# Performance work log

Hardware: AMD Instinct MI355X
Metric: run time of the kernel (lower is better)

## Reference

```python
import jax, jax.numpy as jnp
import numpy as np
from jax import lax

HID = 2048; NK = 16; NV = 32; DK = 128; DV = 128; KSZ = 4; CHUNK = 64; S = 2048
KEY_DIM = NK * DK; VAL_DIM = NV * DV; CONV_DIM = 2 * KEY_DIM + VAL_DIM
EPS = 1e-6


def l2norm(x, eps=1e-6):
    return x * lax.rsqrt((x * x).sum(-1, keepdims=True) + eps)


def chunk_gated_delta_rule(q, k, v, g, beta, chunk=CHUNK):
    # q,k: [B,S,Hv,DK]; v: [B,S,Hv,DV]; g,beta: [B,S,Hv]
    q = l2norm(q); k = l2norm(k)  # use_qk_l2norm_in_kernel=True
    q, k, v = (jnp.swapaxes(x, 1, 2) for x in (q, k, v))  # [B,H,S,D]
    g = jnp.swapaxes(g, 1, 2); beta = jnp.swapaxes(beta, 1, 2)  # [B,H,S]
    B, H, Ssz, Dk = k.shape; Dv = v.shape[-1]
    N = Ssz // chunk  # seq_len chosen divisible by chunk -> pad is no-op
    q = q * (Dk ** -0.5)
    vb = v * beta[..., None]
    kb = k * beta[..., None]
    rs = lambda x: x.reshape(B, H, N, chunk, x.shape[-1])
    q, k, v, kb, vb = map(rs, (q, k, v, kb, vb))
    g = jnp.cumsum(g.reshape(B, H, N, chunk), axis=-1)
    tril = jnp.tril(jnp.ones((chunk, chunk), bool))
    stril = jnp.tril(jnp.ones((chunk, chunk), bool), -1)
    diff = jnp.where(tril, g[..., :, None] - g[..., None, :], 0.0)
    decay_mask = jnp.where(tril, jnp.exp(diff), 0.0)  # [B,H,N,C,C]
    attn = jnp.where(stril, -(kb @ jnp.swapaxes(k, -1, -2)) * decay_mask, 0.0)
    # UT (WY) transform: sequential row updates, scan over in-chunk index
    def ut_body(a, i):
        row = jnp.take(a, i, axis=-2)  # [B,H,N,C]
        new = row + jnp.einsum('bhnk,bhnkj->bhnj', row, a)
        return a.at[:, :, :, i, :].set(new), None
    attn, _ = lax.scan(ut_body, attn, jnp.arange(1, chunk))
    attn = attn + jnp.eye(chunk, dtype=attn.dtype)
    u = attn @ vb                                   # [B,H,N,C,DV]
    kcd = attn @ (kb * jnp.exp(g)[..., None])       # [B,H,N,C,DK]
    init = jnp.zeros((B, H, Dk, Dv), q.dtype)
    def step(state, inp):
        q_i, k_i, u_i, kcd_i, g_i, dm_i = inp
        scores = (q_i @ jnp.swapaxes(k_i, -1, -2)) * dm_i
        v_new = u_i - kcd_i @ state
        inter = (q_i * jnp.exp(g_i)[..., None]) @ state
        o = inter + scores @ v_new
        gl = g_i[..., -1]  # [B,H]
        state = state * jnp.exp(gl)[..., None, None] + jnp.einsum(
            'bhcd,bhce->bhde', k_i * jnp.exp(gl[..., None] - g_i)[..., None], v_new)
        return state, o
    mv = lambda x: jnp.moveaxis(x, 2, 0)
    _, out = lax.scan(step, init, (mv(q), mv(k), mv(u), mv(kcd), mv(g), mv(decay_mask)))
    out = jnp.moveaxis(out, 0, 2).reshape(B, H, Ssz, Dv)
    return jnp.swapaxes(out, 1, 2)  # [B,S,H,DV]


def setup_inputs() -> dict:
    key = jax.random.key(0)
    ks = jax.random.split(key, 8)
    return {
        'hidden_states': jax.random.normal(ks[0], (S, HID), jnp.float32),
        'W_qkv': jax.random.normal(ks[1], (CONV_DIM, HID), jnp.float32) * 0.02,
        'W_z': jax.random.normal(ks[2], (VAL_DIM, HID), jnp.float32) * 0.02,
        'W_a': jax.random.normal(ks[3], (NV, HID), jnp.float32) * 0.02,
        'W_b': jax.random.normal(ks[4], (NV, HID), jnp.float32) * 0.02,
        'conv_w': jax.random.normal(ks[5], (CONV_DIM, 1, KSZ), jnp.float32) * 0.1,
        'dt_bias': jnp.ones((NV,), jnp.float32),
        'A_log': jnp.log(jax.random.uniform(ks[6], (NV,), jnp.float32, 0.1, 16.0)),
        'norm_w': jnp.ones((DV,), jnp.float32),
        'W_out': jax.random.normal(ks[7], (HID, VAL_DIM), jnp.float32) * 0.02,
    }


def reference(hidden_states, W_qkv, W_z, W_a, W_b, conv_w, dt_bias, A_log, norm_w, W_out):
    x = hidden_states  # [S, HID]
    mixed = x @ W_qkv.T  # [S, CONV_DIM]
    z = (x @ W_z.T).reshape(-1, DV)  # [S*NV, DV]
    a = x @ W_a.T  # [S, NV]
    b = x @ W_b.T
    # causal depthwise conv1d (torch pads K-1 both sides then slices [:S])
    conv = lax.conv_general_dilated(
        mixed.T[None], conv_w, (1,), [(KSZ - 1, 0)],
        dimension_numbers=('NCH', 'OIH', 'NCH'), feature_group_count=CONV_DIM)
    mixed = jax.nn.silu(conv[0].T)  # [S, CONV_DIM]
    q = mixed[:, :KEY_DIM].reshape(1, S, NK, DK)
    k = mixed[:, KEY_DIM:2 * KEY_DIM].reshape(1, S, NK, DK)
    v = mixed[:, 2 * KEY_DIM:].reshape(1, S, NV, DV)
    beta = jax.nn.sigmoid(b)[None]  # [1,S,NV]
    g = (-jnp.exp(A_log) * jax.nn.softplus(a + dt_bias))[None]  # [1,S,NV]
    ratio = NV // NK
    q = jnp.repeat(q, ratio, axis=2)
    k = jnp.repeat(k, ratio, axis=2)
    core = chunk_gated_delta_rule(q, k, v, g, beta)  # [1,S,NV,DV]
    h = core.reshape(-1, DV)  # [S*NV, DV]
    var = jnp.mean(h * h, axis=-1, keepdims=True)
    h = h * lax.rsqrt(var + EPS) * norm_w
    h = h * jax.nn.silu(z)
    out = h.reshape(S, VAL_DIM) @ W_out.T  # [S, HID]
    return out
```

## Files before the change

### kernel.cpp

```cpp
#include <hip/hip_runtime.h>
#include <hip/hip_bf16.h>
#include <math.h>

#define S_LEN   2048
#define HIDDIM  2048
#define NKH     16
#define NVH     32
#define DKD     128
#define DVD     128
#define CCH     64
#define NCHK    32
#define KEY_DIM 2048
#define VAL_DIM 4096
#define CONV_DIM 8192

#define PA_LDS_BYTES (16384 + 16384 + 32768 + 4096 + 4096 + 256 + 256 + 256)
#define PB_LDS_BYTES ((2 * 29696 + 2048 + 1024 + 1024) * 2 + 2048 * 4)
#define G256_LDS_BYTES (3 * 16384 * 2)
#define G128_LDS_BYTES (3 * 8192 * 2)

typedef __bf16 bf16x8 __attribute__((ext_vector_type(8)));
typedef float f32x4 __attribute__((ext_vector_type(4)));

__device__ __forceinline__ float sigmoid_f(float x) { return 1.f / (1.f + __expf(-x)); }
__device__ __forceinline__ float silu_f(float x) { return x * sigmoid_f(x); }
__device__ __forceinline__ ushort f2bf(float f) {
    unsigned u = __float_as_uint(f);
    u += 0x7fffu + ((u >> 16) & 1u);
    return (ushort)(u >> 16);
}
__device__ __forceinline__ float bf2f(ushort u) {
    return __uint_as_float((unsigned)u << 16);
}

#define GLL(srcp, dstp) __builtin_amdgcn_global_load_lds( \
    (const __attribute__((address_space(1))) void*)(srcp), \
    (__attribute__((address_space(3))) void*)(dstp), 16, 0, 0)

#define NX8  (S_LEN * HIDDIM / 8)
#define NQ8  (CONV_DIM * HIDDIM / 8)
#define NZ8  (VAL_DIM * HIDDIM / 8)
#define NW8  (HIDDIM * VAL_DIM / 8)
__global__ __launch_bounds__(256) void cast4_kernel(
    const float* __restrict__ x, const float* __restrict__ Wq,
    const float* __restrict__ Wz, const float* __restrict__ Wo,
    ushort* __restrict__ xb, ushort* __restrict__ wqz, ushort* __restrict__ wob)
{
    int t = blockIdx.x * 256 + threadIdx.x;
    const float* src;
    ushort* dst;
    if (t < NX8) { src = x + (size_t)t * 8; dst = xb + (size_t)t * 8; }
    else if (t < NX8 + NQ8) {
        size_t o = (size_t)(t - NX8) * 8;
        src = Wq + o; dst = wqz + o;
    } else if (t < NX8 + NQ8 + NZ8) {
        size_t o = (size_t)(t - NX8 - NQ8) * 8;
        src = Wz + o; dst = wqz + (size_t)NQ8 * 8 + o;
    } else {
        size_t o = (size_t)(t - NX8 - NQ8 - NZ8) * 8;
        src = Wo + o; dst = wob + o;
    }
    float4 v0 = *(const float4*)(src);
    float4 v1 = *(const float4*)(src + 4);
    union { ushort u[8]; uint4 v; } r;
    r.u[0] = f2bf(v0.x); r.u[1] = f2bf(v0.y); r.u[2] = f2bf(v0.z); r.u[3] = f2bf(v0.w);
    r.u[4] = f2bf(v1.x); r.u[5] = f2bf(v1.y); r.u[6] = f2bf(v1.z); r.u[7] = f2bf(v1.w);
    *(uint4*)dst = r.v;
}

__global__ __launch_bounds__(256) void cast_ab_kernel(
    const float* __restrict__ Wa, const float* __restrict__ Wb, ushort* __restrict__ out)
{
    int t = blockIdx.x * 256 + threadIdx.x;
    int row = t >> 8;
    int c8 = (t & 255) * 8;
    union { ushort u[8]; uint4 v; } r;
    if (row < 64) {
        const float* src = (row < 32) ? (Wa + (size_t)row * HIDDIM + c8)
                                      : (Wb + (size_t)(row - 32) * HIDDIM + c8);
        float4 v0 = *(const float4*)(src);
        float4 v1 = *(const float4*)(src + 4);
        r.u[0] = f2bf(v0.x); r.u[1] = f2bf(v0.y); r.u[2] = f2bf(v0.z); r.u[3] = f2bf(v0.w);
        r.u[4] = f2bf(v1.x); r.u[5] = f2bf(v1.y); r.u[6] = f2bf(v1.z); r.u[7] = f2bf(v1.w);
    } else {
        r.u[0] = r.u[1] = r.u[2] = r.u[3] = r.u[4] = r.u[5] = r.u[6] = r.u[7] = 0;
    }
    *(uint4*)(out + (size_t)t * 8) = r.v;
}

__global__ __launch_bounds__(512, 1) void gemm256_kernel(
    const ushort* __restrict__ A, const ushort* __restrict__ B,
    ushort* __restrict__ C0, ushort* __restrict__ C1,
    int K, int NSPLIT, int ldc0, int ldc1)
{
    extern __shared__ ushort g2s[];
    const int tid = threadIdx.x;
    const int wv = tid >> 6, ln = tid & 63;
    const int wm = wv >> 1, wn = wv & 1;
    const int lrow = ln & 15, lkg = ln >> 4;
    const int bm = blockIdx.y * 256, bn = blockIdx.x * 256;

    int soff[2];
#pragma unroll
    for (int j = 0; j < 2; ++j) {
        int g = tid + j * 512;
        int l = g & 63;
        soff[j] = (((g >> 6) * 16) + (l & 15)) * K + (l >> 4) * 8;
    }
    const ushort* Abase = A + (size_t)bm * K;
    const ushort* Bbase = B + (size_t)bn * K;

    f32x4 acc[4][8];
#pragma unroll
    for (int m = 0; m < 4; ++m)
#pragma unroll
        for (int n = 0; n < 8; ++n) {
            f32x4 z = {0.f, 0.f, 0.f, 0.f};
            acc[m][n] = z;
        }

#define G256_STAGE(bb, k0) do {                                            \
        ushort* bufA_ = g2s + (bb) * 16384;                                \
        ushort* bufB_ = bufA_ + 8192;                                      \
        _Pragma("unroll")                                                  \
        for (int j_ = 0; j_ < 2; ++j_) {                                   \
            GLL(Abase + soff[j_] + (k0), bufA_ + (j_ * 512 + wv * 64) * 8);\
            GLL(Bbase + soff[j_] + (k0), bufB_ + (j_ * 512 + wv * 64) * 8);\
        }                                                                  \
    } while (0)

    const int T = K >> 5;
    G256_STAGE(0, 0);
    G256_STAGE(1, 32);
    int bb = 0;
    for (int t = 0; t < T; ++t) {
        if (t + 1 < T) {
            asm volatile("s_waitcnt vmcnt(4)" ::: "memory");
        } else {
            asm volatile("s_waitcnt vmcnt(0)" ::: "memory");
        }
        __builtin_amdgcn_s_barrier();
        if (t + 2 < T) G256_STAGE((bb >= 1) ? (bb - 1) : (bb + 2), (t + 2) * 32);
        const ushort* LA = g2s + bb * 16384;
        const ushort* LB = LA + 8192;
        __builtin_amdgcn_s_setprio(1);
        {
            bf16x8 afv[4], bfv[8];
#pragma unroll
            for (int mf = 0; mf < 4; ++mf)
                afv[mf] = *(const bf16x8*)&LA[((wm * 4 + mf) * 64 + ln) * 8];
#pragma unroll
            for (int nf = 0; nf < 8; ++nf)
                bfv[nf] = *(const bf16x8*)&LB[((wn * 8 + nf) * 64 + ln) * 8];
#pragma unroll
            for (int mf = 0; mf < 4; ++mf)
#pragma unroll
                for (int nf = 0; nf < 8; ++nf)
                    acc[mf][nf] = __builtin_amdgcn_mfma_f32_16x16x32_bf16(
                        afv[mf], bfv[nf], acc[mf][nf], 0, 0, 0);
        }
        __builtin_amdgcn_s_setprio(0);
        bb = (bb == 2) ? 0 : bb + 1;
    }
#undef G256_STAGE

    const bool inC1 = (bn >= NSPLIT);
    ushort* Cp = inC1 ? C1 : C0;
    const int ldc = inC1 ? ldc1 : ldc0;
    const int cboff = bn + wn * 128 - (inC1 ? NSPLIT : 0);
#pragma unroll
    for (int mf = 0; mf < 4; ++mf) {
        const int row0 = bm + wm * 64 + mf * 16 + lkg * 4;
#pragma unroll
        for (int nf = 0; nf < 8; ++nf) {
            ushort* cp = Cp + (size_t)row0 * ldc + cboff + nf * 16 + lrow;
#pragma unroll
            for (int j = 0; j < 4; ++j) cp[(size_t)j * ldc] = f2bf(acc[mf][nf][j]);
        }
    }
}

__global__ __launch_bounds__(256, 2) void gemm128_kernel(
    const ushort* __restrict__ A, const ushort* __restrict__ B,
    float* __restrict__ C, int N, int K)
{
    extern __shared__ ushort g1s[];
    const int tid = threadIdx.x;
    const int wv = tid >> 6, ln = tid & 63;
    const int wm = wv >> 1, wn = wv & 1;
    const int lrow = ln & 15, lkg = ln >> 4;
    const int bm = blockIdx.y * 128, bn = blockIdx.x * 128;

    int soff[2];
#pragma unroll
    for (int j = 0; j < 2; ++j) {
        int g = tid + j * 256;
        int l = g & 63;
        soff[j] = (((g >> 6) * 16) + (l & 15)) * K + (l >> 4) * 8;
    }
    const ushort* Abase = A + (size_t)bm * K;
    const ushort* Bbase = B + (size_t)bn * K;

    f32x4 acc[4][4];
#pragma unroll
    for (int m = 0; m < 4; ++m)
#pragma unroll
        for (int n = 0; n < 4; ++n) {
            f32x4 z = {0.f, 0.f, 0.f, 0.f};
            acc[m][n] = z;
        }

#define G128_STAGE(bb, k0) do {                                            \
        ushort* bufA_ = g1s + (bb) * 8192;                                 \
        ushort* bufB_ = bufA_ + 4096;                                      \
        _Pragma("unroll")                                                  \
        for (int j_ = 0; j_ < 2; ++j_) {                                   \
            GLL(Abase + soff[j_] + (k0), bufA_ + (j_ * 256 + wv * 64) * 8);\
            GLL(Bbase + soff[j_] + (k0), bufB_ + (j_ * 256 + wv * 64) * 8);\
        }                                                                  \
    } while (0)

    const int T = K >> 5;
    G128_STAGE(0, 0);
    G128_STAGE(1, 32);
    int bb = 0;
    for (int t = 0; t < T; ++t) {
        if (t + 1 < T) {
            asm volatile("s_waitcnt vmcnt(4)" ::: "memory");
        } else {
            asm volatile("s_waitcnt vmcnt(0)" ::: "memory");
        }
        __builtin_amdgcn_s_barrier();
        if (t + 2 < T) G128_STAGE((bb >= 1) ? (bb - 1) : (bb + 2), (t + 2) * 32);
        const ushort* LA = g1s + bb * 8192;
        const ushort* LB = LA + 4096;
        __builtin_amdgcn_s_setprio(1);
        {
            bf16x8 afv[4], bfv[4];
#pragma unroll
            for (int mf = 0; mf < 4; ++mf)
                afv[mf] = *(const bf16x8*)&LA[((wm * 4 + mf) * 64 + ln) * 8];
#pragma unroll
            for (int nf = 0; nf < 4; ++nf)
                bfv[nf] = *(const bf16x8*)&LB[((wn * 4 + nf) * 64 + ln) * 8];
#pragma unroll
            for (int mf = 0; mf < 4; ++mf)
#pragma unroll
                for (int nf = 0; nf < 4; ++nf)
                    acc[mf][nf] = __builtin_amdgcn_mfma_f32_16x16x32_bf16(
                        afv[mf], bfv[nf], acc[mf][nf], 0, 0, 0);
        }
        __builtin_amdgcn_s_setprio(0);
        bb = (bb == 2) ? 0 : bb + 1;
    }
#undef G128_STAGE

#pragma unroll
    for (int mf = 0; mf < 4; ++mf) {
        const int row0 = bm + wm * 64 + mf * 16 + lkg * 4;
#pragma unroll
        for (int nf = 0; nf < 4; ++nf) {
            float* cp = C + (size_t)row0 * N + bn + wn * 64 + nf * 16 + lrow;
#pragma unroll
            for (int j = 0; j < 4; ++j) cp[(size_t)j * N] = acc[mf][nf][j];
        }
    }
}

__global__ __launch_bounds__(256) void front_kernel(
    const ushort* __restrict__ pre, const float* __restrict__ cw,
    ushort* __restrict__ qnb, ushort* __restrict__ knb, ushort* __restrict__ vbuf)
{
    __shared__ float stage[4096];
    __shared__ float sums[32];
    __shared__ float scal[32];
    const int s = blockIdx.x;
    const int tid = threadIdx.x;

#pragma unroll
    for (int cg = 0; cg < 8; ++cg) {
        const int c = cg * 1024 + tid * 4;
        float w[4][4];
#pragma unroll
        for (int j = 0; j < 4; ++j) {
            float4 wj = *(const float4*)(cw + (size_t)(c + j) * 4);
            w[j][0] = wj.x; w[j][1] = wj.y; w[j][2] = wj.z; w[j][3] = wj.w;
        }
        float a0 = 0.f, a1 = 0.f, a2 = 0.f, a3 = 0.f;
#pragma unroll
        for (int t = 0; t < 4; ++t) {
            int ss = s - 3 + t;
            if (ss >= 0) {
                uint2 xv = *(const uint2*)(pre + (size_t)ss * CONV_DIM + c);
                a0 = fmaf(bf2f((ushort)xv.x), w[0][t], a0);
                a1 = fmaf(bf2f((ushort)(xv.x >> 16)), w[1][t], a1);
                a2 = fmaf(bf2f((ushort)xv.y), w[2][t], a2);
                a3 = fmaf(bf2f((ushort)(xv.y >> 16)), w[3][t], a3);
            }
        }
        a0 = silu_f(a0); a1 = silu_f(a1); a2 = silu_f(a2); a3 = silu_f(a3);
        if (cg < 4) {
            float4 v4 = make_float4(a0, a1, a2, a3);
            *(float4*)&stage[c] = v4;
            float ss2 = a0 * a0 + a1 * a1 + a2 * a2 + a3 * a3;
#pragma unroll
            for (int m = 1; m < 32; m <<= 1) ss2 += __shfl_xor(ss2, m, 32);
            if ((tid & 31) == 0) sums[c >> 7] = ss2;
        } else {
            union { ushort u2[4]; uint2 v; } p;
            p.u2[0] = f2bf(a0); p.u2[1] = f2bf(a1);
            p.u2[2] = f2bf(a2); p.u2[3] = f2bf(a3);
            *(uint2*)(vbuf + (size_t)s * VAL_DIM + (c - 4096)) = p.v;
        }
    }
    __syncthreads();
    if (tid < 32) {
        float sc = rsqrtf(sums[tid] + 1e-6f);
        if (tid < 16) sc *= 0.08838834764831843f;
        scal[tid] = sc;
    }
    __syncthreads();
#pragma unroll
    for (int j = 0; j < 4; ++j) {
        const int c = j * 1024 + tid * 4;
        float4 v4 = *(const float4*)&stage[c];
        const float sc = scal[c >> 7];
        union { ushort u2[4]; uint2 v; } p;
        p.u2[0] = f2bf(v4.x * sc); p.u2[1] = f2bf(v4.y * sc);
        p.u2[2] = f2bf(v4.z * sc); p.u2[3] = f2bf(v4.w * sc);
        if (c < 2048)
            *(uint2*)(qnb + ((size_t)(s * NKH + (c >> 7))) * DKD + (c & 127)) = p.v;
        else
            *(uint2*)(knb + ((size_t)(s * NKH + ((c >> 7) - 16))) * DKD + (c & 127)) = p.v;
    }
}

__global__ __launch_bounds__(256) void gb_kernel(
    const float* __restrict__ ab, const float* __restrict__ dt_bias,
    const float* __restrict__ A_log, float* __restrict__ g, float* __restrict__ beta)
{
    int idx = blockIdx.x * 256 + threadIdx.x;
    int s = idx >> 5, h = idx & 31;
    float av = ab[(size_t)s * 128 + h] + dt_bias[h];
    float sp = (av > 20.f) ? av : log1pf(__expf(av));
    g[idx] = -__expf(A_log[h]) * sp;
    beta[idx] = sigmoid_f(ab[(size_t)s * 128 + 32 + h]);
}

__global__ __launch_bounds__(256) void phaseA_kernel(
    const ushort* __restrict__ qnb, const ushort* __restrict__ knb,
    const ushort* __restrict__ vbuf, const float* __restrict__ gbuf,
    const float* __restrict__ betabuf,
    ushort* __restrict__ u, ushort* __restrict__ kcd,
    ushort* __restrict__ scores, float* __restrict__ gcs_out,
    ushort* __restrict__ knT)
{
    extern __shared__ char pasm[];
    ushort* kb    = (ushort*)(pasm);
    ushort* qb    = (ushort*)(pasm + 16384);
    ushort* Xb    = (ushort*)(pasm + 32768);
    float*  Adiag = (float*)(pasm + 65536);
    ushort* Ab    = (ushort*)(pasm + 69632);
    float*  gcs_s = (float*)(pasm + 73728);
    float*  bet_s = (float*)(pasm + 73984);
    float*  scK_s = (float*)(pasm + 74240);
    float*  Pf    = (float*)qb;

    const int n = blockIdx.x, h = blockIdx.y, kh = h >> 1;
    const int tid = threadIdx.x;
    const int s0 = n * CCH;
    const int wv = tid >> 6, ln = tid & 63;
    const int lrow = ln & 15, lkg = ln >> 4;

    float xr[64];
    if (tid < 128) {
        const ushort* vp = vbuf + (size_t)s0 * VAL_DIM + h * DVD + tid;
#pragma unroll
        for (int i = 0; i < 64; ++i) xr[i] = bf2f(vp[(size_t)i * VAL_DIM]);
    } else {
        const ushort* kp = knb + ((size_t)s0 * NKH + kh) * DKD + (tid - 128);
#pragma unroll
        for (int i = 0; i < 64; ++i) xr[i] = bf2f(kp[(size_t)i * (NKH * DKD)]);
    }

    {
        uint4 z = {0, 0, 0, 0};
#pragma unroll
        for (int i = 0; i < 8; ++i)
            *(uint4*)&Xb[(i * 256 + tid) * 8] = z;
        *(uint4*)&Ab[tid * 8] = z;
    }

    if (tid < 64) {
        float gv = gbuf[(size_t)(s0 + tid) * NVH + h];
#pragma unroll
        for (int off = 1; off < 64; off <<= 1) {
            float pv = __shfl_up(gv, off, 64);
            if (tid >= off) gv += pv;
        }
        float bv = betabuf[(size_t)(s0 + tid) * NVH + h];
        gcs_s[tid] = gv;
        bet_s[tid] = bv;
        scK_s[tid] = bv * __expf(gv);
        gcs_out[(size_t)h * S_LEN + s0 + tid] = gv;
    }

    {
        const int r = tid >> 2, c0 = (tid & 3) * 32;
        const int mbase = (((r >> 4) * 4 + (tid & 3)) * 64 + (r & 15)) * 8;
        const ushort* ksrc = knb + ((size_t)(s0 + r) * NKH + kh) * DKD + c0;
        const ushort* qsrc = qnb + ((size_t)(s0 + r) * NKH + kh) * DKD + c0;
#pragma unroll
        for (int j0 = 0; j0 < 4; ++j0) {
            *(uint4*)&kb[mbase + (j0 << 7)] = *(const uint4*)(ksrc + j0 * 8);
            *(uint4*)&qb[mbase + (j0 << 7)] = *(const uint4*)(qsrc + j0 * 8);
        }
    }
    __syncthreads();

    f32x4 accA[4], accQ[4];
#pragma unroll
    for (int j = 0; j < 4; ++j) {
        f32x4 z = {0.f, 0.f, 0.f, 0.f};
        accA[j] = z; accQ[j] = z;
    }
#pragma unroll
    for (int ks = 0; ks < 4; ++ks) {
        bf16x8 a_k = *(const bf16x8*)&kb[((wv * 4 + ks) * 64 + ln) * 8];
        bf16x8 a_q = *(const bf16x8*)&qb[((wv * 4 + ks) * 64 + ln) * 8];
#pragma unroll
        for (int j = 0; j < 4; ++j) {
            bf16x8 b_k = *(const bf16x8*)&kb[((j * 4 + ks) * 64 + ln) * 8];
            accA[j] = __builtin_amdgcn_mfma_f32_16x16x32_bf16(a_k, b_k, accA[j], 0, 0, 0);
            accQ[j] = __builtin_amdgcn_mfma_f32_16x16x32_bf16(a_q, b_k, accQ[j], 0, 0, 0);
        }
    }
    {
        ushort* scp = scores + (size_t)(h * NCHK + n) * (CCH * CCH);
#pragma unroll
        for (int j = 0; j < 4; ++j) {
            const int c = j * 16 + lrow;
            const float gc = gcs_s[c];
#pragma unroll
            for (int jj = 0; jj < 4; ++jj) {
                const int i = wv * 16 + lkg * 4 + jj;
                const float e = __expf(gcs_s[i] - gc);
                float sv = (i >= c) ? (accQ[j][jj] * e) : 0.f;
                scp[i * CCH + c] = f2bf(sv);
                float aval = (i > c) ? (-bet_s[i] * accA[j][jj] * e) : 0.f;
                if (j == wv) {
                    Adiag[wv * 256 + (i & 15) * 16 + lrow] = aval;
                } else if (j < wv) {
                    const int f = (wv == 1) ? 0 : ((wv == 2) ? 1 : (2 + (j >> 1)));
                    const int lk = ((j & 1) << 4) | lrow;
                    const int lane2 = (i & 15) | ((lk >> 3) << 4);
                    Ab[(f * 64 + lane2) * 8 + (lk & 7)] = f2bf(aval);
                }
            }
        }
    }
    if (tid < 128) {
#pragma unroll
        for (int i4 = 0; i4 < 16; ++i4) {
            float4 b4 = *(const float4*)&bet_s[i4 * 4];
            xr[i4 * 4 + 0] *= b4.x; xr[i4 * 4 + 1] *= b4.y;
            xr[i4 * 4 + 2] *= b4.z; xr[i4 * 4 + 3] *= b4.w;
        }
    } else {
#pragma unroll
        for (int i4 = 0; i4 < 16; ++i4) {
            float4 b4 = *(const float4*)&scK_s[i4 * 4];
            xr[i4 * 4 + 0] *= b4.x; xr[i4 * 4 + 1] *= b4.y;
            xr[i4 * 4 + 2] *= b4.z; xr[i4 * 4 + 3] *= b4.w;
        }
    }
    __syncthreads();

    const int ct = tid >> 4, lct = tid & 15;
#pragma unroll
    for (int s = 0; s < 4; ++s) {
        float y[16];
        float pr[16];
        if (s > 0) {
#pragma unroll
            for (int r = 0; r < 16; ++r) pr[r] = Pf[r * 256 + tid];
        } else {
#pragma unroll
            for (int r = 0; r < 16; ++r) pr[r] = 0.f;
        }
#pragma unroll
        for (int r = 0; r < 16; ++r) {
            float acc = xr[s * 16 + r] + pr[r];
#pragma unroll
            for (int k4 = 0; k4 < 16; k4 += 4) {
                if (k4 < r) {
                    float4 a4 = *(const float4*)&Adiag[s * 256 + r * 16 + k4];
                    if (k4 + 0 < r) acc = fmaf(a4.x, y[k4 + 0], acc);
                    if (k4 + 1 < r) acc = fmaf(a4.y, y[k4 + 1], acc);
                    if (k4 + 2 < r) acc = fmaf(a4.z, y[k4 + 2], acc);
                    if (k4 + 3 < r) acc = fmaf(a4.w, y[k4 + 3], acc);
                }
            }
            y[r] = acc;
        }
        if (tid < 128) {
            ushort* up = u + (size_t)(h * NCHK + n) * (CCH * DVD) + (s * 16) * DVD + tid;
#pragma unroll
            for (int r = 0; r < 16; ++r) up[r * DVD] = f2bf(y[r]);
        } else {
            ushort* kp = kcd + (size_t)(h * NCHK + n) * (CCH * DKD) + (s * 16) * DKD + (tid - 128);
#pragma unroll
            for (int r = 0; r < 16; ++r) kp[r * DKD] = f2bf(y[r]);
        }
        if (s < 3) {
#pragma unroll
            for (int half = 0; half < 2; ++half) {
                union { ushort us[8]; uint4 v; } p;
#pragma unroll
                for (int e = 0; e < 8; ++e) p.us[e] = f2bf(y[half * 8 + e]);
                const int kg = (s & 1) * 2 + half;
                *(uint4*)&Xb[(((s >> 1) * 16 + ct) * 64 + (kg * 16 + lct)) * 8] = p.v;
            }
            __syncthreads();
            const int snx = s + 1;
            const int nT2 = (snx + 1) >> 1;
            f32x4 accP[4];
#pragma unroll
            for (int ctl = 0; ctl < 4; ++ctl) {
                f32x4 z = {0.f, 0.f, 0.f, 0.f};
                accP[ctl] = z;
            }
#pragma unroll
            for (int t2 = 0; t2 < 2; ++t2) {
                if (t2 < nT2) {
                    const int f = (snx == 1) ? 0 : ((snx == 2) ? 1 : (2 + t2));
                    bf16x8 a = *(const bf16x8*)&Ab[(f * 64 + ln) * 8];
#pragma unroll
                    for (int ctl = 0; ctl < 4; ++ctl) {
                        bf16x8 b = *(const bf16x8*)&Xb[((t2 * 16 + wv * 4 + ctl) * 64 + ln) * 8];
                        accP[ctl] = __builtin_amdgcn_mfma_f32_16x16x32_bf16(a, b, accP[ctl], 0, 0, 0);
                    }
                }
            }
#pragma unroll
            for (int ctl = 0; ctl < 4; ++ctl)
#pragma unroll
                for (int jj = 0; jj < 4; ++jj)
                    Pf[(lkg * 4 + jj) * 256 + wv * 64 + ctl * 16 + lrow] = accP[ctl][jj];
            __syncthreads();
        }
    }

    if (!(h & 1)) {
        const int dk = tid >> 1, ch = (tid & 1) * 32;
        ushort* dst = knT + ((size_t)(kh * NCHK + n) * DKD + dk) * CCH + ch;
        const int kpart = ((dk >> 5) * 64) * 8 + (((dk >> 3) & 3) << 4) * 8 + (dk & 7);
#pragma unroll
        for (int j0 = 0; j0 < 32; j0 += 8) {
            union { ushort us[8]; uint4 v; } p;
#pragma unroll
            for (int j = 0; j < 8; ++j) {
                const int row = ch + j0 + j;
                p.us[j] = kb[((row >> 4) * 4 * 64 + (row & 15)) * 8 + kpart];
            }
            *(uint4*)(dst + j0) = p.v;
        }
    }
}

__global__ __launch_bounds__(256) void phaseB_kernel(
    const ushort* __restrict__ qnb, const ushort* __restrict__ knT,
    const ushort* __restrict__ u, const ushort* __restrict__ kcd,
    const ushort* __restrict__ sc, const float* __restrict__ gcs,
    ushort* __restrict__ obuf)
{
    extern __shared__ ushort smu[];
    ushort* storg  = smu + 59392;
    ushort* vnorg  = smu + 61440;
    ushort* vnsorg = smu + 62464;
    float*  gcsall = (float*)(smu + 63488);

    const int h = blockIdx.x;
    const int dvb = blockIdx.y;
    const int d0 = dvb * 16;
    const int kh = h >> 1;
    const int tid = threadIdx.x;
    const int wv = tid >> 6, ln = tid & 63;
    const int lrow = ln & 15, lkg = ln >> 4;

    {
        uint4 z = {0, 0, 0, 0};
        *(uint4*)&storg[tid * 8] = z;
    }

    const int q_lane  = lrow * (NKH * DKD) + kh * DKD + wv * 32 + lkg * 8;
    const int kc_lane = lrow * DKD + wv * 32 + lkg * 8;
    const int st_lane = ((tid >> 7) * 16 + lrow) * 64 + ((tid >> 6) & 1) * 32 + lkg * 8;
    const int dst_e   = wv * 512;

#define PBSTG(bsel, nn) do {                                                  \
        const ushort* qsrc_  = qnb + (size_t)((nn) * CCH) * (NKH * DKD);      \
        const ushort* kcsrc_ = kcd + (size_t)(h * NCHK + (nn)) * (CCH * DKD); \
        const ushort* scsrc_ = sc  + (size_t)(h * NCHK + (nn)) * (CCH * CCH); \
        const ushort* kTsrc_ = knT + (size_t)(kh * NCHK + (nn)) * (DKD * CCH);\
        const ushort* usrc_  = u   + (size_t)(h * NCHK + (nn)) * (CCH * DVD) + d0; \
        ushort* base_ = smu + (bsel) * 29696;                                 \
        _Pragma("unroll")                                                     \
        for (int r_ = 0; r_ < 4; ++r_) {                                      \
            GLL(qsrc_ + q_lane + r_ * 32768, base_ + r_ * 2048 + dst_e);      \
            GLL(kcsrc_ + kc_lane + r_ * 2048, base_ + 8192 + r_ * 2048 + dst_e); \
            GLL(kTsrc_ + st_lane + r_ * 2048, base_ + 20480 + r_ * 2048 + dst_e); \
        }                                                                     \
        _Pragma("unroll")                                                     \
        for (int r_ = 0; r_ < 2; ++r_)                                        \
            GLL(scsrc_ + st_lane + r_ * 2048, base_ + 16384 + r_ * 2048 + dst_e); \
        if (tid < 128)                                                        \
            GLL(usrc_ + (tid >> 1) * DVD + (tid & 1) * 8, base_ + 28672 + tid * 8); \
    } while (0)

    PBSTG(0, 0);
    {
        float4 g0 = *(const float4*)(gcs + (size_t)h * S_LEN + tid * 8);
        float4 g1 = *(const float4*)(gcs + (size_t)h * S_LEN + tid * 8 + 4);
        *(float4*)&gcsall[tid * 8] = g0;
        *(float4*)&gcsall[tid * 8 + 4] = g1;
    }
    __syncthreads();

    f32x4 accS0 = {0.f, 0.f, 0.f, 0.f}, accS1 = {0.f, 0.f, 0.f, 0.f};

    for (int n = 0; n < NCHK; ++n) {
        const int cur = n & 1;
        if (n + 1 < NCHK) PBSTG(cur ^ 1, n + 1);
        const ushort* qorg  = smu + cur * 29696;
        const ushort* kcorg = qorg + 8192;
        const ushort* scorg = qorg + 16384;
        const ushort* kTorg = qorg + 20480;
        const ushort* uorg  = qorg + 28672;
        const float*  gcs_s = gcsall + n * 64;
        const int s0 = n * CCH;

        f32x4 accv = {0.f, 0.f, 0.f, 0.f};
        f32x4 acco = {0.f, 0.f, 0.f, 0.f};
#pragma unroll
        for (int ks = 0; ks < 4; ++ks) {
            bf16x8 b_st = *(const bf16x8*)&storg[(ks * 64 + ln) * 8];
            bf16x8 a_kc = *(const bf16x8*)&kcorg[((wv * 4 + ks) * 64 + ln) * 8];
            bf16x8 a_q  = *(const bf16x8*)&qorg[((wv * 4 + ks) * 64 + ln) * 8];
            accv = __builtin_amdgcn_mfma_f32_16x16x32_bf16(a_kc, b_st, accv, 0, 0, 0);
            acco = __builtin_amdgcn_mfma_f32_16x16x32_bf16(a_q, b_st, acco, 0, 0, 0);
        }
        const int row = wv * 16 + lkg * 4;
        float u0 = bf2f(uorg[(row + 0) * 16 + lrow]);
        float u1 = bf2f(uorg[(row + 1) * 16 + lrow]);
        float u2 = bf2f(uorg[(row + 2) * 16 + lrow]);
        float u3 = bf2f(uorg[(row + 3) * 16 + lrow]);
        const float gl = gcs_s[63];
        float vn0 = u0 - accv[0], vn1 = u1 - accv[1];
        float vn2 = u2 - accv[2], vn3 = u3 - accv[3];
        {
            float g0 = gcs_s[row], g1 = gcs_s[row + 1], g2 = gcs_s[row + 2], g3 = gcs_s[row + 3];
            acco[0] *= __expf(g0); acco[1] *= __expf(g1);
            acco[2] *= __expf(g2); acco[3] *= __expf(g3);
            const int eb = ((wv >> 1) * 64 + ((wv & 1) * 2 + (lkg >> 1)) * 16 + lrow) * 8
                         + (lkg & 1) * 4;
            union { ushort u2a[4]; uint2 v; } pa, pb;
            pa.u2a[0] = f2bf(vn0); pa.u2a[1] = f2bf(vn1);
            pa.u2a[2] = f2bf(vn2); pa.u2a[3] = f2bf(vn3);
            pb.u2a[0] = f2bf(vn0 * __expf(gl - g0)); pb.u2a[1] = f2bf(vn1 * __expf(gl - g1));
            pb.u2a[2] = f2bf(vn2 * __expf(gl - g2)); pb.u2a[3] = f2bf(vn3 * __expf(gl - g3));
            *(uint2*)&vnorg[eb] = pa.v;
            *(uint2*)&vnsorg[eb] = pb.v;
        }
        __syncthreads();

#pragma unroll
        for (int ks = 0; ks < 2; ++ks) {
            bf16x8 a_sc = *(const bf16x8*)&scorg[((wv * 2 + ks) * 64 + ln) * 8];
            bf16x8 b_vn = *(const bf16x8*)&vnorg[(ks * 64 + ln) * 8];
            acco = __builtin_amdgcn_mfma_f32_16x16x32_bf16(a_sc, b_vn, acco, 0, 0, 0);
        }
        ushort* op = obuf + (size_t)(s0 + row) * VAL_DIM + h * DVD + d0 + lrow;
        op[0] = f2bf(acco[0]); op[VAL_DIM] = f2bf(acco[1]);
        op[2 * VAL_DIM] = f2bf(acco[2]); op[3 * VAL_DIM] = f2bf(acco[3]);

        const float egl = __expf(gl);
        accS0 *= egl; accS1 *= egl;
#pragma unroll
        for (int ks = 0; ks < 2; ++ks) {
            bf16x8 a_vs = *(const bf16x8*)&vnsorg[(ks * 64 + ln) * 8];
            bf16x8 b_k0 = *(const bf16x8*)&kTorg[(((wv * 2 + 0) * 2 + ks) * 64 + ln) * 8];
            bf16x8 b_k1 = *(const bf16x8*)&kTorg[(((wv * 2 + 1) * 2 + ks) * 64 + ln) * 8];
            accS0 = __builtin_amdgcn_mfma_f32_16x16x32_bf16(a_vs, b_k0, accS0, 0, 0, 0);
            accS1 = __builtin_amdgcn_mfma_f32_16x16x32_bf16(a_vs, b_k1, accS1, 0, 0, 0);
        }
#pragma unroll
        for (int j = 0; j < 4; ++j) {
            storg[(wv * 64 + ((lrow >> 3)) * 16 + lkg * 4 + j) * 8 + (lrow & 7)] = f2bf(accS0[j]);
            storg[(wv * 64 + (2 + (lrow >> 3)) * 16 + lkg * 4 + j) * 8 + (lrow & 7)] = f2bf(accS1[j]);
        }
        __syncthreads();
    }
#undef PBSTG
}

__global__ __launch_bounds__(256) void norm_kernel(
    const ushort* __restrict__ obuf, const ushort* __restrict__ z,
    const float* __restrict__ nw, ushort* __restrict__ hbuf)
{
    int row = (blockIdx.x * 256 + threadIdx.x) >> 6;
    int lane = threadIdx.x & 63;
    uint ov = *(const uint*)(obuf + (size_t)row * DVD + lane * 2);
    float x0 = bf2f((ushort)ov), x1 = bf2f((ushort)(ov >> 16));
    float ss = x0 * x0 + x1 * x1;
#pragma unroll
    for (int m = 1; m < 64; m <<= 1) ss += __shfl_xor(ss, m, 64);
    float scale = rsqrtf(ss * (1.f / DVD) + 1e-6f);
    uint zv = *(const uint*)(z + (size_t)row * DVD + lane * 2);
    float z0 = bf2f((ushort)zv), z1 = bf2f((ushort)(zv >> 16));
    float2 w2 = *(const float2*)(nw + lane * 2);
    float h0 = x0 * scale * w2.x * silu_f(z0);
    float h1 = x1 * scale * w2.y * silu_f(z1);
    union { ushort u[2]; uint v; } r;
    r.u[0] = f2bf(h0); r.u[1] = f2bf(h1);
    *(uint*)(hbuf + (size_t)row * DVD + lane * 2) = r.v;
}

extern "C" void kernel_launch(void* const* d_in, const int* in_sizes, int n_in,
                              void* d_out, int out_size, void* d_ws, size_t ws_size,
                              hipStream_t stream)
{
    (void)in_sizes; (void)n_in; (void)out_size; (void)ws_size;
    const float* x      = (const float*)d_in[0];
    const float* W_qkv  = (const float*)d_in[1];
    const float* W_z    = (const float*)d_in[2];
    const float* W_a    = (const float*)d_in[3];
    const float* W_b    = (const float*)d_in[4];
    const float* conv_w = (const float*)d_in[5];
    const float* dt_b   = (const float*)d_in[6];
    const float* A_log  = (const float*)d_in[7];
    const float* norm_w = (const float*)d_in[8];
    const float* W_out  = (const float*)d_in[9];
    float* out = (float*)d_out;

    char* ws = (char*)d_ws;
    ushort* mixed_pre = (ushort*)(ws);
    ushort* u_buf     = (ushort*)(ws);
    ushort* kcd_buf   = (ushort*)(ws + 33554432);
    ushort* knT_buf   = (ushort*)(ws + 50331648);
    ushort* wqz       = (ushort*)(ws + 67108864);
    ushort* xb        = (ushort*)(ws + 117440512);
    ushort* vbuf      = (ushort*)(ws + 67108864);
    ushort* obuf      = (ushort*)(ws + 83886080);
    ushort* hbuf      = (ushort*)(ws + 100663296);
    ushort* z_buf     = (ushort*)(ws + 134217728);
    ushort* sc_buf    = (ushort*)(ws + 167772160);
    ushort* wabb      = (ushort*)(ws + 167772160);
    float*  ab_buf    = (float*)(ws + 168296448);
    ushort* qnb       = (ushort*)(ws + 176160768);
    ushort* knb       = (ushort*)(ws + 184549376);
    float*  g_buf     = (float*)(ws + 201326592);
    float*  bet_buf   = (float*)(ws + 201588736);
    float*  gcs_buf   = (float*)(ws + 201850880);
    ushort* wob       = (ushort*)(ws + 202113024);

    hipFuncSetAttribute((const void*)phaseA_kernel,
                        hipFuncAttributeMaxDynamicSharedMemorySize, PA_LDS_BYTES);
    hipFuncSetAttribute((const void*)phaseB_kernel,
                        hipFuncAttributeMaxDynamicSharedMemorySize, PB_LDS_BYTES);
    hipFuncSetAttribute((const void*)gemm256_kernel,
                        hipFuncAttributeMaxDynamicSharedMemorySize, G256_LDS_BYTES);
    hipFuncSetAttribute((const void*)gemm128_kernel,
                        hipFuncAttributeMaxDynamicSharedMemorySize, G128_LDS_BYTES);

    dim3 blk(256);
    cast4_kernel<<<(NX8 + NQ8 + NZ8 + NW8) / 256, blk, 0, stream>>>(
        x, W_qkv, W_z, W_out, xb, wqz, wob);
    cast_ab_kernel<<<(128 * HIDDIM / 8) / 256, blk, 0, stream>>>(W_a, W_b, wabb);
    gemm256_kernel<<<dim3((CONV_DIM + VAL_DIM) / 256, S_LEN / 256), dim3(512), G256_LDS_BYTES, stream>>>(
        xb, wqz, mixed_pre, z_buf, HIDDIM, CONV_DIM, CONV_DIM, VAL_DIM);
    gemm128_kernel<<<dim3(1, S_LEN / 128), blk, G128_LDS_BYTES, stream>>>(
        xb, wabb, ab_buf, 128, HIDDIM);
    front_kernel<<<S_LEN, blk, 0, stream>>>(mixed_pre, conv_w, qnb, knb, vbuf);
    gb_kernel<<<(S_LEN * NVH) / 256, blk, 0, stream>>>(ab_buf, dt_b, A_log, g_buf, bet_buf);
    phaseA_kernel<<<dim3(NCHK, NVH), blk, PA_LDS_BYTES, stream>>>(
        qnb, knb, vbuf, g_buf, bet_buf, u_buf, kcd_buf, sc_buf, gcs_buf, knT_buf);
    phaseB_kernel<<<dim3(NVH, 8), blk, PB_LDS_BYTES, stream>>>(
        qnb, knT_buf, u_buf, kcd_buf, sc_buf, gcs_buf, obuf);
    norm_kernel<<<(S_LEN * NVH * 64) / 256, blk, 0, stream>>>(obuf, z_buf, norm_w, hbuf);
    gemm128_kernel<<<dim3(HIDDIM / 128, S_LEN / 128), blk, G128_LDS_BYTES, stream>>>(
        hbuf, wob, out, HIDDIM, VAL_DIM);
}
```

Before: 440.9 us.

## Fold a/b projection into big QKVZ GEMM and merge cast kernels

The W_a/W_b casts are folded into the main cast kernel, and the a/b projection is appended as an extra 256-column tile to the large QKVZ GEMM. That GEMM gains a third fp32 output region and a block-index swizzle over the 49x8 grid. This removes two kernel launches and the small, poorly occupied 128-wide GEMM. The cost is zero-padding the a/b weight block to 256 rows and relying on wab sitting contiguously after wqz in the workspace so the B operand spans both.

```diff
diff --git a/kernel.cpp b/kernel.cpp
--- a/kernel.cpp
+++ b/kernel.cpp
@@ -41,10 +41,13 @@
 #define NQ8  (CONV_DIM * HIDDIM / 8)
 #define NZ8  (VAL_DIM * HIDDIM / 8)
 #define NW8  (HIDDIM * VAL_DIM / 8)
-__global__ __launch_bounds__(256) void cast4_kernel(
+#define NA8  (256 * HIDDIM / 8)
+__global__ __launch_bounds__(256) void cast5_kernel(
     const float* __restrict__ x, const float* __restrict__ Wq,
     const float* __restrict__ Wz, const float* __restrict__ Wo,
-    ushort* __restrict__ xb, ushort* __restrict__ wqz, ushort* __restrict__ wob)
+    const float* __restrict__ Wa, const float* __restrict__ Wb,
+    ushort* __restrict__ xb, ushort* __restrict__ wqz, ushort* __restrict__ wob,
+    ushort* __restrict__ wab)
 {
     int t = blockIdx.x * 256 + threadIdx.x;
     const float* src;
@@ -56,9 +59,21 @@
     } else if (t < NX8 + NQ8 + NZ8) {
         size_t o = (size_t)(t - NX8 - NQ8) * 8;
         src = Wz + o; dst = wqz + (size_t)NQ8 * 8 + o;
-    } else {
+    } else if (t < NX8 + NQ8 + NZ8 + NW8) {
         size_t o = (size_t)(t - NX8 - NQ8 - NZ8) * 8;
         src = Wo + o; dst = wob + o;
+    } else {
+        int g = t - NX8 - NQ8 - NZ8 - NW8;
+        int row = g >> 8;
+        int c8 = (g & 255) * 8;
+        dst = wab + (size_t)g * 8;
+        if (row >= 64) {
+            uint4 z = {0, 0, 0, 0};
+            *(uint4*)dst = z;
+            return;
+        }
+        src = (row < 32) ? (Wa + (size_t)row * HIDDIM + c8)
+                         : (Wb + (size_t)(row - 32) * HIDDIM + c8);
     }
     float4 v0 = *(const float4*)(src);
     float4 v1 = *(const float4*)(src + 4);
@@ -68,37 +83,19 @@
     *(uint4*)dst = r.v;
 }
 
-__global__ __launch_bounds__(256) void cast_ab_kernel(
-    const float* __restrict__ Wa, const float* __restrict__ Wb, ushort* __restrict__ out)
-{
-    int t = blockIdx.x * 256 + threadIdx.x;
-    int row = t >> 8;
-    int c8 = (t & 255) * 8;
-    union { ushort u[8]; uint4 v; } r;
-    if (row < 64) {
-        const float* src = (row < 32) ? (Wa + (size_t)row * HIDDIM + c8)
-                                      : (Wb + (size_t)(row - 32) * HIDDIM + c8);
-        float4 v0 = *(const float4*)(src);
-        float4 v1 = *(const float4*)(src + 4);
-        r.u[0] = f2bf(v0.x); r.u[1] = f2bf(v0.y); r.u[2] = f2bf(v0.z); r.u[3] = f2bf(v0.w);
-        r.u[4] = f2bf(v1.x); r.u[5] = f2bf(v1.y); r.u[6] = f2bf(v1.z); r.u[7] = f2bf(v1.w);
-    } else {
-        r.u[0] = r.u[1] = r.u[2] = r.u[3] = r.u[4] = r.u[5] = r.u[6] = r.u[7] = 0;
-    }
-    *(uint4*)(out + (size_t)t * 8) = r.v;
-}
-
 __global__ __launch_bounds__(512, 1) void gemm256_kernel(
     const ushort* __restrict__ A, const ushort* __restrict__ B,
-    ushort* __restrict__ C0, ushort* __restrict__ C1,
-    int K, int NSPLIT, int ldc0, int ldc1)
+    ushort* __restrict__ C0, ushort* __restrict__ C1, float* __restrict__ C2,
+    int K, int NS1, int NS2, int ldc0, int ldc1, int ldc2)
 {
     extern __shared__ ushort g2s[];
     const int tid = threadIdx.x;
     const int wv = tid >> 6, ln = tid & 63;
     const int wm = wv >> 1, wn = wv & 1;
     const int lrow = ln & 15, lkg = ln >> 4;
-    const int bm = blockIdx.y * 256, bn = blockIdx.x * 256;
+    const int bid = blockIdx.y * 49 + blockIdx.x;
+    const int swz = (bid & 7) * 49 + (bid >> 3);
+    const int bm = (swz / 49) * 256, bn = (swz % 49) * 256;
 
     int soff[2];
 #pragma unroll
@@ -164,18 +161,32 @@
     }
 #undef G256_STAGE
 
-    const bool inC1 = (bn >= NSPLIT);
-    ushort* Cp = inC1 ? C1 : C0;
-    const int ldc = inC1 ? ldc1 : ldc0;
-    const int cboff = bn + wn * 128 - (inC1 ? NSPLIT : 0);
-#pragma unroll
-    for (int mf = 0; mf < 4; ++mf) {
-        const int row0 = bm + wm * 64 + mf * 16 + lkg * 4;
-#pragma unroll
-        for (int nf = 0; nf < 8; ++nf) {
-            ushort* cp = Cp + (size_t)row0 * ldc + cboff + nf * 16 + lrow;
-#pragma unroll
-            for (int j = 0; j < 4; ++j) cp[(size_t)j * ldc] = f2bf(acc[mf][nf][j]);
+    if (bn < NS2) {
+        const bool inC1 = (bn >= NS1);
+        ushort* Cp = inC1 ? C1 : C0;
+        const int ldc = inC1 ? ldc1 : ldc0;
+        const int cboff = bn + wn * 128 - (inC1 ? NS1 : 0);
+#pragma unroll
+        for (int mf = 0; mf < 4; ++mf) {
+            const int row0 = bm + wm * 64 + mf * 16 + lkg * 4;
+#pragma unroll
+            for (int nf = 0; nf < 8; ++nf) {
+                ushort* cp = Cp + (size_t)row0 * ldc + cboff + nf * 16 + lrow;
+#pragma unroll
+                for (int j = 0; j < 4; ++j) cp[(size_t)j * ldc] = f2bf(acc[mf][nf][j]);
+            }
+        }
+    } else {
+        const int cboff = bn + wn * 128 - NS2;
+#pragma unroll
+        for (int mf = 0; mf < 4; ++mf) {
+            const int row0 = bm + wm * 64 + mf * 16 + lkg * 4;
+#pragma unroll
+            for (int nf = 0; nf < 8; ++nf) {
+                float* cp = C2 + (size_t)row0 * ldc2 + cboff + nf * 16 + lrow;
+#pragma unroll
+                for (int j = 0; j < 4; ++j) cp[(size_t)j * ldc2] = acc[mf][nf][j];
+            }
         }
     }
 }
@@ -341,10 +352,10 @@
 {
     int idx = blockIdx.x * 256 + threadIdx.x;
     int s = idx >> 5, h = idx & 31;
-    float av = ab[(size_t)s * 128 + h] + dt_bias[h];
+    float av = ab[(size_t)s * 256 + h] + dt_bias[h];
     float sp = (av > 20.f) ? av : log1pf(__expf(av));
     g[idx] = -__expf(A_log[h]) * sp;
-    beta[idx] = sigmoid_f(ab[(size_t)s * 128 + 32 + h]);
+    beta[idx] = sigmoid_f(ab[(size_t)s * 256 + 32 + h]);
 }
 
 __global__ __launch_bounds__(256) void phaseA_kernel(
@@ -749,14 +760,14 @@
     ushort* kcd_buf   = (ushort*)(ws + 33554432);
     ushort* knT_buf   = (ushort*)(ws + 50331648);
     ushort* wqz       = (ushort*)(ws + 67108864);
-    ushort* xb        = (ushort*)(ws + 117440512);
+    ushort* wab       = (ushort*)(ws + 117440512);
+    ushort* xb        = (ushort*)(ws + 118489088);
     ushort* vbuf      = (ushort*)(ws + 67108864);
     ushort* obuf      = (ushort*)(ws + 83886080);
     ushort* hbuf      = (ushort*)(ws + 100663296);
     ushort* z_buf     = (ushort*)(ws + 134217728);
     ushort* sc_buf    = (ushort*)(ws + 167772160);
-    ushort* wabb      = (ushort*)(ws + 167772160);
-    float*  ab_buf    = (float*)(ws + 168296448);
+    float*  ab_buf    = (float*)(ws + 167772160);
     ushort* qnb       = (ushort*)(ws + 176160768);
     ushort* knb       = (ushort*)(ws + 184549376);
     float*  g_buf     = (float*)(ws + 201326592);
@@ -774,13 +785,11 @@
                         hipFuncAttributeMaxDynamicSharedMemorySize, G128_LDS_BYTES);
 
     dim3 blk(256);
-    cast4_kernel<<<(NX8 + NQ8 + NZ8 + NW8) / 256, blk, 0, stream>>>(
-        x, W_qkv, W_z, W_out, xb, wqz, wob);
-    cast_ab_kernel<<<(128 * HIDDIM / 8) / 256, blk, 0, stream>>>(W_a, W_b, wabb);
-    gemm256_kernel<<<dim3((CONV_DIM + VAL_DIM) / 256, S_LEN / 256), dim3(512), G256_LDS_BYTES, stream>>>(
-        xb, wqz, mixed_pre, z_buf, HIDDIM, CONV_DIM, CONV_DIM, VAL_DIM);
-    gemm128_kernel<<<dim3(1, S_LEN / 128), blk, G128_LDS_BYTES, stream>>>(
-        xb, wabb, ab_buf, 128, HIDDIM);
+    cast5_kernel<<<(NX8 + NQ8 + NZ8 + NW8 + NA8) / 256, blk, 0, stream>>>(
+        x, W_qkv, W_z, W_out, W_a, W_b, xb, wqz, wob, wab);
+    gemm256_kernel<<<dim3(49, S_LEN / 256), dim3(512), G256_LDS_BYTES, stream>>>(
+        xb, wqz, mixed_pre, z_buf, ab_buf, HIDDIM,
+        CONV_DIM, CONV_DIM + VAL_DIM, CONV_DIM, VAL_DIM, 256);
     front_kernel<<<S_LEN, blk, 0, stream>>>(mixed_pre, conv_w, qnb, knb, vbuf);
     gb_kernel<<<(S_LEN * NVH) / 256, blk, 0, stream>>>(ab_buf, dt_b, A_log, g_buf, bet_buf);
     phaseA_kernel<<<dim3(NCHK, NVH), blk, PA_LDS_BYTES, stream>>>(
```

After: 408.5 us. -7.3%, faster.
